# Kernel tuning notes

Hardware: AMD Instinct MI355X
Metric: run time of the kernel (lower is better)

The kernel has to match this reference:

```python
import jax, jax.numpy as jnp
import numpy as np
from jax import lax

EPS = 1e-5
NUM_HEADS = 8


def _safe_norm(x):
    # sqrt(max(sum x^2, EPS^2)) == max(||x||, EPS); grad-safe at 0
    return jnp.sqrt(jnp.maximum(jnp.sum(x * x, axis=-1, keepdims=True), EPS * EPS))


def _project(x):
    norm = _safe_norm(x)
    max_norm = 1.0 - EPS
    scale = jnp.where(norm >= max_norm, max_norm / (norm + EPS), jnp.ones_like(norm))
    return x * scale


def _logmap0(y):
    # logarithmic_map(0, y): lambda_0 = 2/(1+EPS)
    y = _project(y)
    n = _safe_norm(y)  # clamp(min=EPS) is built in
    lam = 2.0 / (1.0 + EPS)
    return (2.0 / lam) * jnp.arctanh(n) * (y / n)


def _expmap0(v):
    # exponential_map(0, v): lambda_0 = 2/(1+EPS)
    n = _safe_norm(v)
    lam = 2.0 / (1.0 + EPS)
    return _project(jnp.tanh(lam * n / 2.0) * (v / n))


def _mobius_add(x, y):
    x = _project(x)
    y = _project(y)
    xy = jnp.sum(x * y, axis=-1, keepdims=True)
    xn = jnp.sum(x * x, axis=-1, keepdims=True)
    yn = jnp.sum(y * y, axis=-1, keepdims=True)
    num = (1.0 + 2.0 * xy + yn) * x + (1.0 - xn) * y
    den = 1.0 + 2.0 * xy + xn * yn + EPS
    return _project(num / den)


def _hyp_linear(x, W, b):
    # HyperbolicLinear.forward: project -> logmap0 -> linear -> expmap0 -> mobius-add bias
    x = _project(x)
    xt = _logmap0(x)
    t = xt @ W.T
    r = _expmap0(t)
    r = _mobius_add(r, jnp.broadcast_to(b, r.shape))
    return r


def setup_inputs() -> dict:
    key = jax.random.key(0)
    ks = jax.random.split(key, 11)
    B, S, E = 4, 512, 512

    def xavier(k, shape):
        bound = np.sqrt(6.0 / (shape[0] + shape[1]))
        return jax.random.uniform(k, shape, jnp.float32, -bound, bound)

    return {
        "query": jax.random.normal(ks[0], (B, S, E), jnp.float32),
        "key": jax.random.normal(ks[1], (B, S, E), jnp.float32),
        "value": jax.random.normal(ks[2], (B, S, E), jnp.float32),
        "Wq": xavier(ks[3], (E, E)), "bq": 0.01 * jax.random.normal(ks[4], (E,), jnp.float32),
        "Wk": xavier(ks[5], (E, E)), "bk": 0.01 * jax.random.normal(ks[6], (E,), jnp.float32),
        "Wv": xavier(ks[7], (E, E)), "bv": 0.01 * jax.random.normal(ks[8], (E,), jnp.float32),
        "Wo": xavier(ks[9], (E, E)), "bo": 0.01 * jax.random.normal(ks[10], (E,), jnp.float32),
    }


def reference(query, key, value, Wq, bq, Wk, bk, Wv, bv, Wo, bo):
    B, S, E = query.shape
    H = NUM_HEADS
    D = E // H

    Q = _hyp_linear(query, Wq, bq).reshape(B, S, H, D).transpose(0, 2, 1, 3)  # [B,H,S,D]
    K = _hyp_linear(key, Wk, bk).reshape(B, S, H, D).transpose(0, 2, 1, 3)
    V = _hyp_linear(value, Wv, bv).reshape(B, S, H, D).transpose(0, 2, 1, 3)

    # Pairwise Poincare distance: d(q,k) = acosh(1 + 2||q-k||^2/((1-|q|^2)(1-|k|^2)) + EPS)
    q = _project(Q)
    k = _project(K)
    qn = jnp.sum(q * q, axis=-1)  # [B,H,S]
    kn = jnp.sum(k * k, axis=-1)  # [B,H,S]
    qk = jnp.einsum('bhqd,bhkd->bhqk', q, k)
    num = jnp.maximum(qn[..., :, None] + kn[..., None, :] - 2.0 * qk, 0.0)
    den = jnp.maximum((1.0 - qn)[..., :, None] * (1.0 - kn)[..., None, :], EPS)
    dist = jnp.arccosh(1.0 + 2.0 * num / den + EPS)  # [B,H,Sq,Sk]
    attn = jax.nn.softmax(-dist, axis=-1)

    # Sequential Mobius-add accumulation over key/value positions
    wt = jnp.moveaxis(attn, 3, 0)  # [Sk,B,H,Sq]
    vt = jnp.moveaxis(V, 2, 0)     # [Sk,B,H,D]

    @jax.checkpoint
    def step(ws, wv):
        wj, vj = wv  # wj: [B,H,Sq], vj: [B,H,D]
        return _mobius_add(ws, wj[..., None] * vj[:, :, None, :]), None

    ws0 = jnp.zeros((B, H, S, D), query.dtype)
    attended, _ = lax.scan(step, ws0, (wt, vt))  # [B,H,Sq,D]

    attended = attended.transpose(0, 2, 1, 3).reshape(B, S, E)
    return _hyp_linear(attended, Wo, bo)
```

## Files before the change

### kernel.cpp

```cpp
#include <hip/hip_runtime.h>
#include <math.h>

#define EPS  1e-5f
#define EPS2 1e-10f
#define MAXN (1.0f - EPS)

using short8  = __attribute__((ext_vector_type(8))) short;
using floatx4 = __attribute__((ext_vector_type(4))) float;
using float2v = __attribute__((ext_vector_type(2))) float;

template <int CTRL>
static __device__ __forceinline__ float qperm(float x) {
  return __int_as_float(__builtin_amdgcn_update_dpp(
      __float_as_int(x), __float_as_int(x), CTRL, 0xF, 0xF, false));
}
#define QP_XOR1    0xB1
#define QP_XOR2    0x4E
#define QP_HALFMIR 0x141

#if __has_builtin(__builtin_elementwise_fma)
static __device__ __forceinline__ float2v fma2(float2v a, float2v b, float2v c) {
  return __builtin_elementwise_fma(a, b, c);
}
#else
static __device__ __forceinline__ float2v fma2(float2v a, float2v b, float2v c) {
  float2v r; r.x = fmaf(a.x, b.x, c.x); r.y = fmaf(a.y, b.y, c.y); return r;
}
#endif

static __device__ __forceinline__ int pack_hi2(float a, float b) {
  return (int)((__float_as_uint(a) >> 16) | (__float_as_uint(b) & 0xFFFF0000u));
}
static __device__ __forceinline__ float hi_of(float a) {
  return __uint_as_float(__float_as_uint(a) & 0xFFFF0000u);
}

static __device__ __forceinline__ float logmap_f(float ss) {
  const float r = sqrtf(fmaxf(ss, EPS2));
  float at;
  if (r >= MAXN) {
    at = 0.5f * logf((r * (2.0f - EPS) + EPS) / (EPS * (1.0f + r)));
  } else {
    at = 0.5f * logf((1.0f + r) / (1.0f - r));
  }
  return (1.0f + EPS) * at / r;
}

__global__ __launch_bounds__(256) void k_gemm_mfma(
    const float* __restrict__ A0, const float* __restrict__ A1, const float* __restrict__ A2,
    const float* __restrict__ W0, const float* __restrict__ W1, const float* __restrict__ W2,
    float* __restrict__ Cbase) {
  const int z = blockIdx.z;
  const float* A = (z == 0) ? A0 : ((z == 1) ? A1 : A2);
  const float* W = (z == 0) ? W0 : ((z == 1) ? W1 : W2);
  float* C = Cbase + (size_t)z * (2048 * 512);
  __shared__ int Ahi[64][36], Alo[64][36], Whi[64][36], Wlo[64][36];
  __shared__ float f_lds[64];
  const int t = threadIdx.x;
  const int n0 = blockIdx.x * 64;
  const int m0 = blockIdx.y * 64;
  const int row = t >> 2, c0 = (t & 3) * 16, ci = (t & 3) * 8;
  const int w = t >> 6, lane = t & 63;
  const int quad = lane >> 4, l16 = lane & 15;
  const int mw = (w & 1) * 32, nw = (w >> 1) * 32;
  floatx4 acc[2][2];
#pragma unroll
  for (int i = 0; i < 2; ++i)
#pragma unroll
    for (int j = 0; j < 2; ++j) acc[i][j] = (floatx4){0.f, 0.f, 0.f, 0.f};
  float ssq = 0.0f;

  for (int k0 = 0; k0 < 512; k0 += 64) {
    float4 av[4], wv[4];
#pragma unroll
    for (int i = 0; i < 4; ++i) {
      av[i] = *(const float4*)&A[(size_t)(n0 + row) * 512 + k0 + c0 + 4 * i];
      wv[i] = *(const float4*)&W[(size_t)(m0 + row) * 512 + k0 + c0 + 4 * i];
    }
    int pAh[8], pAl[8], pWh[8], pWl[8];
#pragma unroll
    for (int i = 0; i < 4; ++i) {
      ssq = fmaf(av[i].x, av[i].x, ssq); ssq = fmaf(av[i].y, av[i].y, ssq);
      ssq = fmaf(av[i].z, av[i].z, ssq); ssq = fmaf(av[i].w, av[i].w, ssq);
      pAh[2 * i]     = pack_hi2(av[i].x, av[i].y);
      pAh[2 * i + 1] = pack_hi2(av[i].z, av[i].w);
      pAl[2 * i]     = pack_hi2(av[i].x - hi_of(av[i].x), av[i].y - hi_of(av[i].y));
      pAl[2 * i + 1] = pack_hi2(av[i].z - hi_of(av[i].z), av[i].w - hi_of(av[i].w));
      pWh[2 * i]     = pack_hi2(wv[i].x, wv[i].y);
      pWh[2 * i + 1] = pack_hi2(wv[i].z, wv[i].w);
      pWl[2 * i]     = pack_hi2(wv[i].x - hi_of(wv[i].x), wv[i].y - hi_of(wv[i].y));
      pWl[2 * i + 1] = pack_hi2(wv[i].z - hi_of(wv[i].z), wv[i].w - hi_of(wv[i].w));
    }
    __syncthreads();
    *(int4*)&Ahi[row][ci]     = *(int4*)&pAh[0];
    *(int4*)&Ahi[row][ci + 4] = *(int4*)&pAh[4];
    *(int4*)&Alo[row][ci]     = *(int4*)&pAl[0];
    *(int4*)&Alo[row][ci + 4] = *(int4*)&pAl[4];
    *(int4*)&Whi[row][ci]     = *(int4*)&pWh[0];
    *(int4*)&Whi[row][ci + 4] = *(int4*)&pWh[4];
    *(int4*)&Wlo[row][ci]     = *(int4*)&pWl[0];
    *(int4*)&Wlo[row][ci + 4] = *(int4*)&pWl[4];
    __syncthreads();
#pragma unroll
    for (int kk = 0; kk < 64; kk += 32) {
      short8 ah[2], al[2], bh[2], bl[2];
#pragma unroll
      for (int i = 0; i < 2; ++i) {
        ah[i] = *(const short8*)&((const short*)Ahi[mw + i * 16 + l16])[kk + quad * 8];
        al[i] = *(const short8*)&((const short*)Alo[mw + i * 16 + l16])[kk + quad * 8];
        bh[i] = *(const short8*)&((const short*)Whi[nw + i * 16 + l16])[kk + quad * 8];
        bl[i] = *(const short8*)&((const short*)Wlo[nw + i * 16 + l16])[kk + quad * 8];
      }
#pragma unroll
      for (int i = 0; i < 2; ++i)
#pragma unroll
        for (int j = 0; j < 2; ++j) {
          acc[i][j] = __builtin_amdgcn_mfma_f32_16x16x32_bf16(ah[i], bh[j], acc[i][j], 0, 0, 0);
          acc[i][j] = __builtin_amdgcn_mfma_f32_16x16x32_bf16(ah[i], bl[j], acc[i][j], 0, 0, 0);
          acc[i][j] = __builtin_amdgcn_mfma_f32_16x16x32_bf16(al[i], bh[j], acc[i][j], 0, 0, 0);
        }
    }
  }
  ssq += qperm<QP_XOR1>(ssq);
  ssq += qperm<QP_XOR2>(ssq);
  if ((t & 3) == 0) f_lds[row] = logmap_f(ssq);
  __syncthreads();
#pragma unroll
  for (int i = 0; i < 2; ++i) {
    const int lrow_base = mw + i * 16 + quad * 4;
#pragma unroll
    for (int r = 0; r < 4; ++r) {
      const float fv = f_lds[lrow_base + r];
#pragma unroll
      for (int j = 0; j < 2; ++j)
        C[(size_t)(n0 + lrow_base + r) * 512 + m0 + nw + j * 16 + l16] = fv * acc[i][j][r];
    }
  }
}

__global__ __launch_bounds__(256) void k_post(const float* __restrict__ tin,
                                              const float* __restrict__ b0,
                                              const float* __restrict__ b1,
                                              const float* __restrict__ b2,
                                              float* __restrict__ o0, float* __restrict__ o1,
                                              float* __restrict__ o2,
                                              float* __restrict__ nrm0, float* __restrict__ nrm1,
                                              float* __restrict__ nrm2,
                                              float* __restrict__ rowsum_init, int final_mode) {
  const int nrow = blockIdx.x, z = blockIdx.y, t = threadIdx.x;
  const float* tv = tin + ((size_t)z * 2048 + nrow) * 512;
  const float* bias = (z == 0) ? b0 : ((z == 1) ? b1 : b2);
  const int e0 = 2 * t;
  const float2 tp = *(const float2*)&tv[e0];
  const float2 bp = *(const float2*)&bias[e0];
  float p_tt = tp.x * tp.x + tp.y * tp.y;
  float p_tb = tp.x * bp.x + tp.y * bp.y;
  float p_bb = bp.x * bp.x + bp.y * bp.y;
#pragma unroll
  for (int m = 32; m; m >>= 1) {
    p_tt += __shfl_xor(p_tt, m, 64);
    p_tb += __shfl_xor(p_tb, m, 64);
    p_bb += __shfl_xor(p_bb, m, 64);
  }
  __shared__ float red[4][3];
  const int lane = t & 63, w = t >> 6;
  if (lane == 0) { red[w][0] = p_tt; red[w][1] = p_tb; red[w][2] = p_bb; }
  __syncthreads();
  const float s_tt = red[0][0] + red[1][0] + red[2][0] + red[3][0];
  const float s_tb = red[0][1] + red[1][1] + red[2][1] + red[3][1];
  const float s_bb = red[0][2] + red[1][2] + red[2][2] + red[3][2];
  const float tn = sqrtf(fmaxf(s_tt, EPS2));
  const float th = tanhf(tn / (1.0f + EPS));
  const float g = th / tn;
  const float rnorm = th * (sqrtf(s_tt) / tn);
  const float sr = (rnorm >= MAXN) ? (MAXN / (rnorm + EPS)) : 1.0f;
  const float gr = g * sr;
  const float rn = (rnorm * sr) * (rnorm * sr);
  const float bnorm = sqrtf(fmaxf(s_bb, EPS2));
  const float sb = (bnorm >= MAXN) ? (MAXN / (bnorm + EPS)) : 1.0f;
  const float xy = gr * sb * s_tb;
  const float yn = (sb * sb) * s_bb;
  const float Af = 1.0f + 2.0f * xy + yn;
  const float Cf = 1.0f - rn;
  const float den = 1.0f + 2.0f * xy + rn * yn + EPS;
  const float id = 1.0f / den;
  const float on_raw = (Af * Af * rn + 2.0f * Af * Cf * xy + Cf * Cf * yn) * (id * id);
  const float no = sqrtf(fmaxf(on_raw, EPS2));
  const float so = (no >= MAXN) ? (MAXN / (no + EPS)) : 1.0f;
  const float ms = id * so;
  const float ca = gr * Af * ms;
  const float cb = sb * Cf * ms;
  const float v0 = ca * tp.x + cb * bp.x;
  const float v1 = ca * tp.y + cb * bp.y;
  if (final_mode) {
    float2 o; o.x = v0; o.y = v1;
    *(float2*)&o0[(size_t)nrow * 512 + e0] = o;
    return;
  }
  float hp = v0 * v0 + v1 * v1;
#pragma unroll
  for (int m = 16; m; m >>= 1) hp += __shfl_xor(hp, m, 64);
  const float hnr = sqrtf(fmaxf(hp, EPS2));
  float sh = 1.0f;
  if (z != 2) sh = (hnr >= MAXN) ? (MAXN / (hnr + EPS)) : 1.0f;
  float* outz = (z == 0) ? o0 : ((z == 1) ? o1 : o2);
  float* nz = (z == 0) ? nrm0 : ((z == 1) ? nrm1 : nrm2);
  const int b = nrow >> 9, s = nrow & 511, h = e0 >> 6, d = e0 & 63;
  float2 o; o.x = v0 * sh; o.y = v1 * sh;
  *(float2*)&outz[(((size_t)(b * 8 + h) * 512 + s) * 64 + d)] = o;
  if ((t & 31) == 0) nz[(size_t)(b * 8 + h) * 512 + s] = hp * sh * sh;
  if (z == 0 && t < 8) rowsum_init[((size_t)(nrow >> 9) * 8 + t) * 512 + (nrow & 511)] = 0.0f;
}

__global__ __launch_bounds__(256) void k_logits(const float* __restrict__ Q,
                                                const float* __restrict__ K,
                                                const float* __restrict__ qn,
                                                const float* __restrict__ kn,
                                                float* __restrict__ attn,
                                                float* __restrict__ rowsum) {
  const int bh = blockIdx.z;
  const int i0 = blockIdx.x * 64;
  const int j0 = blockIdx.y * 64;
  const float* Qb = Q + (size_t)bh * 512 * 64;
  const float* Kb = K + (size_t)bh * 512 * 64;
  __shared__ int Qhi[64][36], Qlo[64][36], Khi[64][36], Klo[64][36];
  const int t = threadIdx.x;
  const int row = t >> 2, c0 = (t & 3) * 16, ci = (t & 3) * 8;
  const int w = t >> 6, lane = t & 63;
  const int quad = lane >> 4, l16 = lane & 15;
  const int mw = (w & 1) * 32, nw = (w >> 1) * 32;
  float4 qv4[4], kv4[4];
#pragma unroll
  for (int i = 0; i < 4; ++i) {
    qv4[i] = *(const float4*)&Qb[(size_t)(i0 + row) * 64 + c0 + 4 * i];
    kv4[i] = *(const float4*)&Kb[(size_t)(j0 + row) * 64 + c0 + 4 * i];
  }
  int pQh[8], pQl[8], pKh[8], pKl[8];
#pragma unroll
  for (int i = 0; i < 4; ++i) {
    pQh[2 * i]     = pack_hi2(qv4[i].x, qv4[i].y);
    pQh[2 * i + 1] = pack_hi2(qv4[i].z, qv4[i].w);
    pQl[2 * i]     = pack_hi2(qv4[i].x - hi_of(qv4[i].x), qv4[i].y - hi_of(qv4[i].y));
    pQl[2 * i + 1] = pack_hi2(qv4[i].z - hi_of(qv4[i].z), qv4[i].w - hi_of(qv4[i].w));
    pKh[2 * i]     = pack_hi2(kv4[i].x, kv4[i].y);
    pKh[2 * i + 1] = pack_hi2(kv4[i].z, kv4[i].w);
    pKl[2 * i]     = pack_hi2(kv4[i].x - hi_of(kv4[i].x), kv4[i].y - hi_of(kv4[i].y));
    pKl[2 * i + 1] = pack_hi2(kv4[i].z - hi_of(kv4[i].z), kv4[i].w - hi_of(kv4[i].w));
  }
  *(int4*)&Qhi[row][ci]     = *(int4*)&pQh[0];
  *(int4*)&Qhi[row][ci + 4] = *(int4*)&pQh[4];
  *(int4*)&Qlo[row][ci]     = *(int4*)&pQl[0];
  *(int4*)&Qlo[row][ci + 4] = *(int4*)&pQl[4];
  *(int4*)&Khi[row][ci]     = *(int4*)&pKh[0];
  *(int4*)&Khi[row][ci + 4] = *(int4*)&pKh[4];
  *(int4*)&Klo[row][ci]     = *(int4*)&pKl[0];
  *(int4*)&Klo[row][ci + 4] = *(int4*)&pKl[4];
  __syncthreads();
  floatx4 acc[2][2];
#pragma unroll
  for (int i = 0; i < 2; ++i)
#pragma unroll
    for (int j = 0; j < 2; ++j) acc[i][j] = (floatx4){0.f, 0.f, 0.f, 0.f};
#pragma unroll
  for (int kk = 0; kk < 64; kk += 32) {
    short8 ah[2], al[2], bhv[2], blv[2];
#pragma unroll
    for (int i = 0; i < 2; ++i) {
      ah[i]  = *(const short8*)&((const short*)Qhi[mw + i * 16 + l16])[kk + quad * 8];
      al[i]  = *(const short8*)&((const short*)Qlo[mw + i * 16 + l16])[kk + quad * 8];
      bhv[i] = *(const short8*)&((const short*)Khi[nw + i * 16 + l16])[kk + quad * 8];
      blv[i] = *(const short8*)&((const short*)Klo[nw + i * 16 + l16])[kk + quad * 8];
    }
#pragma unroll
    for (int i = 0; i < 2; ++i)
#pragma unroll
      for (int j = 0; j < 2; ++j) {
        acc[i][j] = __builtin_amdgcn_mfma_f32_16x16x32_bf16(ah[i], bhv[j], acc[i][j], 0, 0, 0);
        acc[i][j] = __builtin_amdgcn_mfma_f32_16x16x32_bf16(ah[i], blv[j], acc[i][j], 0, 0, 0);
        acc[i][j] = __builtin_amdgcn_mfma_f32_16x16x32_bf16(al[i], bhv[j], acc[i][j], 0, 0, 0);
      }
  }
#pragma unroll
  for (int i = 0; i < 2; ++i) {
    float rs_acc[4] = {0.f, 0.f, 0.f, 0.f};
#pragma unroll
    for (int r = 0; r < 4; ++r) {
      const int grow = i0 + mw + i * 16 + quad * 4 + r;
      const float qni = qn[(size_t)bh * 512 + grow];
      const float rq = 1.0f - qni;
#pragma unroll
      for (int j = 0; j < 2; ++j) {
        const int gcol = j0 + nw + j * 16 + l16;
        const float knj = kn[(size_t)bh * 512 + gcol];
        const float num = fmaxf(qni + knj - 2.0f * acc[i][j][r], 0.0f);
        const float den = fmaxf(rq * (1.0f - knj), EPS);
        const float wv = fmaf(2.0f * num, __builtin_amdgcn_rcpf(den), EPS);
        const float s_ = 1.0f + wv + sqrtf(wv * (wv + 2.0f));
        const float rr = __builtin_amdgcn_rcpf(s_);
        rs_acc[r] += rr;
        attn[((size_t)bh * 512 + grow) * 512 + gcol] = rr;
      }
    }
#pragma unroll
    for (int r = 0; r < 4; ++r) {
      float v = rs_acc[r];
      v += __shfl_xor(v, 1, 64); v += __shfl_xor(v, 2, 64);
      v += __shfl_xor(v, 4, 64); v += __shfl_xor(v, 8, 64);
      if (l16 == 0)
        atomicAdd(&rowsum[(size_t)bh * 512 + i0 + mw + i * 16 + quad * 4 + r], v);
    }
  }
}

__global__ __launch_bounds__(256) void k_scan(const float* __restrict__ V,
                                              const float* __restrict__ vn,
                                              const float* __restrict__ rw,
                                              const float* __restrict__ rowsum,
                                              float* __restrict__ att) {
  __shared__ __align__(16) float v_lds[64 * 64];
  __shared__ __align__(16) float sy_lds[32][132];
  __shared__ __align__(16) float g_lds[256];
  const int blk = blockIdx.x;
  const int bh = blk >> 4;
  const int i0 = (blk & 15) * 32;
  const int t = threadIdx.x;
  const int lane = t & 63, w = t >> 6;
  const int row_blk = w * 8 + (lane >> 3);
  const int sub = lane & 7;
  const int d0 = sub * 8;
  const float* Vb = V + (size_t)bh * 512 * 64;
  const float* vnb = vn + (size_t)bh * 512;
  const float* arow = rw + ((size_t)bh * 512 + i0 + row_blk) * 512;
  const float inv_s = __builtin_amdgcn_rcpf(rowsum[(size_t)bh * 512 + i0 + row_blk]);

  {
    const float* vp = Vb + (size_t)(2 * t) * 64;
    float acc = 0.0f;
#pragma unroll
    for (int i = 0; i < 16; ++i) {
      const float4 x = *(const float4*)&vp[4 * i];
      const float4 y = *(const float4*)&vp[64 + 4 * i];
      acc = fmaf(x.x, y.x, acc); acc = fmaf(x.y, y.y, acc);
      acc = fmaf(x.z, y.z, acc); acc = fmaf(x.w, y.w, acc);
    }
    g_lds[t] = acc;
  }

  float2v wsv[4];
#pragma unroll
  for (int k = 0; k < 4; ++k) wsv[k] = (float2v){0.f, 0.f};
  float xn = 0.0f;

  for (int jc = 0; jc < 512; jc += 64) {
#pragma unroll
    for (int it = 0; it < 4; ++it) {
      const int idx4 = it * 256 + t;
      *(float4*)&v_lds[idx4 * 4] = *(const float4*)&Vb[(size_t)jc * 64 + idx4 * 4];
    }
    const float4 a0 = *(const float4*)&arow[jc + sub * 8];
    const float4 a1 = *(const float4*)&arow[jc + sub * 8 + 4];
    const float4 n0 = *(const float4*)&vnb[jc + sub * 8];
    const float4 n1 = *(const float4*)&vnb[jc + sub * 8 + 4];
    const float wq[8] = {a0.x, a0.y, a0.z, a0.w, a1.x, a1.y, a1.z, a1.w};
    const float nq[8] = {n0.x, n0.y, n0.z, n0.w, n1.x, n1.y, n1.z, n1.w};
#pragma unroll
    for (int k = 0; k < 4; ++k) {
      const float s0 = wq[2 * k] * inv_s;
      const float s1 = wq[2 * k + 1] * inv_s;
      float4 pkt;
      pkt.x = s0; pkt.y = (s0 * s0) * nq[2 * k];
      pkt.z = s1; pkt.w = (s1 * s1) * nq[2 * k + 1];
      *(float4*)&sy_lds[row_blk][sub * 16 + 4 * k] = pkt;
    }
    __syncthreads();

#pragma unroll
    for (int p = 0; p < 32; ++p) {
      const int j = 2 * p;
      const float4 sy4 = *(const float4*)&sy_lds[row_blk][4 * p];
      const float gj = g_lds[(jc >> 1) + p];
      const float4 va0 = *(const float4*)&v_lds[j * 64 + d0];
      const float4 va1 = *(const float4*)&v_lds[j * 64 + d0 + 4];
      const float4 vb0 = *(const float4*)&v_lds[(j + 1) * 64 + d0];
      const float4 vb1 = *(const float4*)&v_lds[(j + 1) * 64 + d0 + 4];
      const float2v a0v = {va0.x, va0.y}, a1v = {va0.z, va0.w};
      const float2v a2v = {va1.x, va1.y}, a3v = {va1.z, va1.w};
      const float2v b0v = {vb0.x, vb0.y}, b1v = {vb0.z, vb0.w};
      const float2v b2v = {vb1.x, vb1.y}, b3v = {vb1.z, vb1.w};
      float2v pa = wsv[0] * a0v; pa = fma2(wsv[1], a1v, pa);
      float2v pb = wsv[2] * a2v; pb = fma2(wsv[3], a3v, pb);
      float2v qa = wsv[0] * b0v; qa = fma2(wsv[1], b1v, qa);
      float2v qb = wsv[2] * b2v; qb = fma2(wsv[3], b3v, qb);
      const float2v ps = pa + pb;
      const float2v qs = qa + qb;
      float dd = ps.x + ps.y;
      float ee = qs.x + qs.y;
      dd += qperm<QP_XOR1>(dd);    ee += qperm<QP_XOR1>(ee);
      dd += qperm<QP_XOR2>(dd);    ee += qperm<QP_XOR2>(ee);
      dd += qperm<QP_HALFMIR>(dd); ee += qperm<QP_HALFMIR>(ee);
      const float sw0 = sy4.x, yn0 = sy4.y;
      const float xy0  = sw0 * dd;
      const float den0 = fmaf(2.0f, xy0, fmaf(xn, yn0, 1.0f + EPS));
      const float s20  = fmaf(2.0f, xy0, xn + yn0);
      const float Af0  = fmaf(2.0f, xy0, 1.0f + yn0);
      const float id0  = __builtin_amdgcn_rcpf(den0);
      const float am0  = Af0 * id0;
      const float cm0  = ((1.0f - xn) * sw0) * id0;
      const float xn1  = (s20 * id0) * ((den0 - EPS) * id0);
      const float sw1 = sy4.z, yn1 = sy4.w;
      const float dd1  = fmaf(am0, ee, cm0 * gj);
      const float xy1  = sw1 * dd1;
      const float den1 = fmaf(2.0f, xy1, fmaf(xn1, yn1, 1.0f + EPS));
      const float s21  = fmaf(2.0f, xy1, xn1 + yn1);
      const float Af1  = fmaf(2.0f, xy1, 1.0f + yn1);
      const float id1  = __builtin_amdgcn_rcpf(den1);
      const float am1  = Af1 * id1;
      const float cm1  = ((1.0f - xn1) * sw1) * id1;
      xn = (s21 * id1) * ((den1 - EPS) * id1);
      const float A2 = am1 * am0, Bc = am1 * cm0;
      const float2v A2v = {A2, A2}, Bv = {Bc, Bc}, Cv = {cm1, cm1};
      wsv[0] = fma2(A2v, wsv[0], fma2(Bv, a0v, Cv * b0v));
      wsv[1] = fma2(A2v, wsv[1], fma2(Bv, a1v, Cv * b1v));
      wsv[2] = fma2(A2v, wsv[2], fma2(Bv, a2v, Cv * b2v));
      wsv[3] = fma2(A2v, wsv[3], fma2(Bv, a3v, Cv * b3v));
    }
    __syncthreads();
  }
  const int b = bh >> 3, h = bh & 7;
  float* o = att + (((size_t)b * 512 + i0 + row_blk) * 512 + h * 64 + d0);
  float4 s0; s0.x = wsv[0].x; s0.y = wsv[0].y; s0.z = wsv[1].x; s0.w = wsv[1].y;
  float4 s1; s1.x = wsv[2].x; s1.y = wsv[2].y; s1.z = wsv[3].x; s1.w = wsv[3].y;
  *(float4*)&o[0] = s0;
  *(float4*)&o[4] = s1;
}

extern "C" void kernel_launch(void* const* d_in, const int* in_sizes, int n_in,
                              void* d_out, int out_size, void* d_ws, size_t ws_size,
                              hipStream_t stream) {
  const float* query = (const float*)d_in[0];
  const float* key_  = (const float*)d_in[1];
  const float* value = (const float*)d_in[2];
  const float* Wq = (const float*)d_in[3];
  const float* bq = (const float*)d_in[4];
  const float* Wk = (const float*)d_in[5];
  const float* bk = (const float*)d_in[6];
  const float* Wv = (const float*)d_in[7];
  const float* bv = (const float*)d_in[8];
  const float* Wo = (const float*)d_in[9];
  const float* bo = (const float*)d_in[10];
  float* ws = (float*)d_ws;
  const size_t M = 1u << 20;
  float* Qb     = ws;
  float* Kb     = ws + 1 * M;
  float* Vb     = ws + 2 * M;
  float* qn     = ws + 3 * M;
  float* kn     = qn + 16384;
  float* vn     = kn + 16384;
  float* rowsum = vn + 16384;
  float* rw     = ws + 4 * M;
  float* t3     = ws + 12 * M;
  float* att    = ws + 15 * M;
  float* to_    = ws + 16 * M;

  k_gemm_mfma<<<dim3(32, 8, 3), 256, 0, stream>>>(query, key_, value, Wq, Wk, Wv, t3);
  k_post<<<dim3(2048, 3), 256, 0, stream>>>(t3, bq, bk, bv, Qb, Kb, Vb, qn, kn, vn,
                                            rowsum, 0);
  k_logits<<<dim3(8, 8, 32), 256, 0, stream>>>(Qb, Kb, qn, kn, rw, rowsum);
  k_scan<<<512, 256, 0, stream>>>(Vb, vn, rw, rowsum, att);
  k_gemm_mfma<<<dim3(32, 8, 1), 256, 0, stream>>>(att, att, att, Wo, Wo, Wo, to_);
  k_post<<<dim3(2048, 1), 256, 0, stream>>>(to_, bo, bo, bo, (float*)d_out,
                                            nullptr, nullptr, nullptr, nullptr, nullptr,
                                            nullptr, 1);
}
```

Before: 247.1 us.

## Block the Mobius scan four steps at a time using in-chunk Gram dot products

The sequential Mobius-add scan now advances four key positions per iteration instead of two. The four dot products with the running state are computed up front and reduced in one batch of DPP shuffles, then corrected step by step using pairwise V Gram entries that are built in LDS for each chunk. The old global-memory precompute of adjacent-pair dots is replaced by a per-chunk computation on 96 threads, which adds a barrier. The goal is fewer cross-lane reduction rounds and more instruction-level parallelism along the serial dependency chain, at the cost of more registers and a longer scalar recurrence per step.

```diff
diff --git a/kernel.cpp b/kernel.cpp
--- a/kernel.cpp
+++ b/kernel.cpp
@@ -318,8 +318,8 @@
                                               const float* __restrict__ rowsum,
                                               float* __restrict__ att) {
   __shared__ __align__(16) float v_lds[64 * 64];
-  __shared__ __align__(16) float sy_lds[32][132];
-  __shared__ __align__(16) float g_lds[256];
+  __shared__ __align__(16) float sy_lds[32 * 132];
+  __shared__ __align__(16) float g_lds[16 * 8];
   const int blk = blockIdx.x;
   const int bh = blk >> 4;
   const int i0 = (blk & 15) * 32;
@@ -333,19 +333,6 @@
   const float* arow = rw + ((size_t)bh * 512 + i0 + row_blk) * 512;
   const float inv_s = __builtin_amdgcn_rcpf(rowsum[(size_t)bh * 512 + i0 + row_blk]);
 
-  {
-    const float* vp = Vb + (size_t)(2 * t) * 64;
-    float acc = 0.0f;
-#pragma unroll
-    for (int i = 0; i < 16; ++i) {
-      const float4 x = *(const float4*)&vp[4 * i];
-      const float4 y = *(const float4*)&vp[64 + 4 * i];
-      acc = fmaf(x.x, y.x, acc); acc = fmaf(x.y, y.y, acc);
-      acc = fmaf(x.z, y.z, acc); acc = fmaf(x.w, y.w, acc);
-    }
-    g_lds[t] = acc;
-  }
-
   float2v wsv[4];
 #pragma unroll
   for (int k = 0; k < 4; ++k) wsv[k] = (float2v){0.f, 0.f};
@@ -357,72 +344,143 @@
       const int idx4 = it * 256 + t;
       *(float4*)&v_lds[idx4 * 4] = *(const float4*)&Vb[(size_t)jc * 64 + idx4 * 4];
     }
-    const float4 a0 = *(const float4*)&arow[jc + sub * 8];
-    const float4 a1 = *(const float4*)&arow[jc + sub * 8 + 4];
-    const float4 n0 = *(const float4*)&vnb[jc + sub * 8];
-    const float4 n1 = *(const float4*)&vnb[jc + sub * 8 + 4];
-    const float wq[8] = {a0.x, a0.y, a0.z, a0.w, a1.x, a1.y, a1.z, a1.w};
-    const float nq[8] = {n0.x, n0.y, n0.z, n0.w, n1.x, n1.y, n1.z, n1.w};
-#pragma unroll
-    for (int k = 0; k < 4; ++k) {
-      const float s0 = wq[2 * k] * inv_s;
-      const float s1 = wq[2 * k + 1] * inv_s;
-      float4 pkt;
-      pkt.x = s0; pkt.y = (s0 * s0) * nq[2 * k];
-      pkt.z = s1; pkt.w = (s1 * s1) * nq[2 * k + 1];
-      *(float4*)&sy_lds[row_blk][sub * 16 + 4 * k] = pkt;
+    {
+      const float4 a0 = *(const float4*)&arow[jc + sub * 8];
+      const float4 a1 = *(const float4*)&arow[jc + sub * 8 + 4];
+      const float4 n0 = *(const float4*)&vnb[jc + sub * 8];
+      const float4 n1 = *(const float4*)&vnb[jc + sub * 8 + 4];
+      const float s0 = a0.x * inv_s, s1 = a0.y * inv_s, s2_ = a0.z * inv_s, s3 = a0.w * inv_s;
+      const float s4 = a1.x * inv_s, s5 = a1.y * inv_s, s6 = a1.z * inv_s, s7 = a1.w * inv_s;
+      float4 p0, p1, p2, p3;
+      p0.x = s0;  p0.y = (s0 * s0) * n0.x;  p0.z = s1;  p0.w = (s1 * s1) * n0.y;
+      p1.x = s2_; p1.y = (s2_ * s2_) * n0.z; p1.z = s3; p1.w = (s3 * s3) * n0.w;
+      p2.x = s4;  p2.y = (s4 * s4) * n1.x;  p2.z = s5;  p2.w = (s5 * s5) * n1.y;
+      p3.x = s6;  p3.y = (s6 * s6) * n1.z;  p3.z = s7;  p3.w = (s7 * s7) * n1.w;
+      const int base = row_blk * 132 + 16 * sub;
+      *(float4*)&sy_lds[base]      = p0;
+      *(float4*)&sy_lds[base + 4]  = p1;
+      *(float4*)&sy_lds[base + 8]  = p2;
+      *(float4*)&sy_lds[base + 12] = p3;
     }
     __syncthreads();
-
-#pragma unroll
-    for (int p = 0; p < 32; ++p) {
-      const int j = 2 * p;
-      const float4 sy4 = *(const float4*)&sy_lds[row_blk][4 * p];
-      const float gj = g_lds[(jc >> 1) + p];
+    if (t < 96) {
+      const int c = t / 6, pi = t - 6 * c;
+      const int kk = (pi < 3) ? 0 : ((pi < 5) ? 1 : 2);
+      const int jj = (pi < 3) ? (pi + 1) : ((pi < 5) ? (pi - 2) : 3);
+      const float* va = &v_lds[(4 * c + kk) * 64];
+      const float* vb = &v_lds[(4 * c + jj) * 64];
+      float acc = 0.0f;
+#pragma unroll
+      for (int i = 0; i < 16; ++i) {
+        const float4 x = *(const float4*)&va[4 * i];
+        const float4 y = *(const float4*)&vb[4 * i];
+        acc = fmaf(x.x, y.x, acc); acc = fmaf(x.y, y.y, acc);
+        acc = fmaf(x.z, y.z, acc); acc = fmaf(x.w, y.w, acc);
+      }
+      g_lds[c * 8 + pi] = acc;
+    }
+    __syncthreads();
+
+    for (int c = 0; c < 16; ++c) {
+      const int j = 4 * c;
+      const float4 sy_a = *(const float4*)&sy_lds[row_blk * 132 + 8 * c];
+      const float4 sy_b = *(const float4*)&sy_lds[row_blk * 132 + 8 * c + 4];
+      const float4 g_a = *(const float4*)&g_lds[c * 8];
+      const float4 g_b = *(const float4*)&g_lds[c * 8 + 4];
       const float4 va0 = *(const float4*)&v_lds[j * 64 + d0];
       const float4 va1 = *(const float4*)&v_lds[j * 64 + d0 + 4];
       const float4 vb0 = *(const float4*)&v_lds[(j + 1) * 64 + d0];
       const float4 vb1 = *(const float4*)&v_lds[(j + 1) * 64 + d0 + 4];
+      const float4 vc0 = *(const float4*)&v_lds[(j + 2) * 64 + d0];
+      const float4 vc1 = *(const float4*)&v_lds[(j + 2) * 64 + d0 + 4];
+      const float4 vd0 = *(const float4*)&v_lds[(j + 3) * 64 + d0];
+      const float4 vd1 = *(const float4*)&v_lds[(j + 3) * 64 + d0 + 4];
       const float2v a0v = {va0.x, va0.y}, a1v = {va0.z, va0.w};
       const float2v a2v = {va1.x, va1.y}, a3v = {va1.z, va1.w};
       const float2v b0v = {vb0.x, vb0.y}, b1v = {vb0.z, vb0.w};
       const float2v b2v = {vb1.x, vb1.y}, b3v = {vb1.z, vb1.w};
+      const float2v c0v = {vc0.x, vc0.y}, c1v = {vc0.z, vc0.w};
+      const float2v c2v = {vc1.x, vc1.y}, c3v = {vc1.z, vc1.w};
+      const float2v d0v = {vd0.x, vd0.y}, d1v = {vd0.z, vd0.w};
+      const float2v d2v = {vd1.x, vd1.y}, d3v = {vd1.z, vd1.w};
       float2v pa = wsv[0] * a0v; pa = fma2(wsv[1], a1v, pa);
       float2v pb = wsv[2] * a2v; pb = fma2(wsv[3], a3v, pb);
+      const float2v sva = pa + pb;
+      float p0 = sva.x + sva.y;
       float2v qa = wsv[0] * b0v; qa = fma2(wsv[1], b1v, qa);
       float2v qb = wsv[2] * b2v; qb = fma2(wsv[3], b3v, qb);
-      const float2v ps = pa + pb;
-      const float2v qs = qa + qb;
-      float dd = ps.x + ps.y;
-      float ee = qs.x + qs.y;
-      dd += qperm<QP_XOR1>(dd);    ee += qperm<QP_XOR1>(ee);
-      dd += qperm<QP_XOR2>(dd);    ee += qperm<QP_XOR2>(ee);
-      dd += qperm<QP_HALFMIR>(dd); ee += qperm<QP_HALFMIR>(ee);
-      const float sw0 = sy4.x, yn0 = sy4.y;
-      const float xy0  = sw0 * dd;
-      const float den0 = fmaf(2.0f, xy0, fmaf(xn, yn0, 1.0f + EPS));
-      const float s20  = fmaf(2.0f, xy0, xn + yn0);
-      const float Af0  = fmaf(2.0f, xy0, 1.0f + yn0);
-      const float id0  = __builtin_amdgcn_rcpf(den0);
-      const float am0  = Af0 * id0;
-      const float cm0  = ((1.0f - xn) * sw0) * id0;
-      const float xn1  = (s20 * id0) * ((den0 - EPS) * id0);
-      const float sw1 = sy4.z, yn1 = sy4.w;
-      const float dd1  = fmaf(am0, ee, cm0 * gj);
-      const float xy1  = sw1 * dd1;
-      const float den1 = fmaf(2.0f, xy1, fmaf(xn1, yn1, 1.0f + EPS));
-      const float s21  = fmaf(2.0f, xy1, xn1 + yn1);
-      const float Af1  = fmaf(2.0f, xy1, 1.0f + yn1);
-      const float id1  = __builtin_amdgcn_rcpf(den1);
-      const float am1  = Af1 * id1;
-      const float cm1  = ((1.0f - xn1) * sw1) * id1;
-      xn = (s21 * id1) * ((den1 - EPS) * id1);
-      const float A2 = am1 * am0, Bc = am1 * cm0;
-      const float2v A2v = {A2, A2}, Bv = {Bc, Bc}, Cv = {cm1, cm1};
-      wsv[0] = fma2(A2v, wsv[0], fma2(Bv, a0v, Cv * b0v));
-      wsv[1] = fma2(A2v, wsv[1], fma2(Bv, a1v, Cv * b1v));
-      wsv[2] = fma2(A2v, wsv[2], fma2(Bv, a2v, Cv * b2v));
-      wsv[3] = fma2(A2v, wsv[3], fma2(Bv, a3v, Cv * b3v));
+      const float2v svb = qa + qb;
+      float p1 = svb.x + svb.y;
+      float2v ra = wsv[0] * c0v; ra = fma2(wsv[1], c1v, ra);
+      float2v rb = wsv[2] * c2v; rb = fma2(wsv[3], c3v, rb);
+      const float2v svc = ra + rb;
+      float p2 = svc.x + svc.y;
+      float2v sa = wsv[0] * d0v; sa = fma2(wsv[1], d1v, sa);
+      float2v sb = wsv[2] * d2v; sb = fma2(wsv[3], d3v, sb);
+      const float2v svd = sa + sb;
+      float p3 = svd.x + svd.y;
+      p0 += qperm<QP_XOR1>(p0); p1 += qperm<QP_XOR1>(p1);
+      p2 += qperm<QP_XOR1>(p2); p3 += qperm<QP_XOR1>(p3);
+      p0 += qperm<QP_XOR2>(p0); p1 += qperm<QP_XOR2>(p1);
+      p2 += qperm<QP_XOR2>(p2); p3 += qperm<QP_XOR2>(p3);
+      p0 += qperm<QP_HALFMIR>(p0); p1 += qperm<QP_HALFMIR>(p1);
+      p2 += qperm<QP_HALFMIR>(p2); p3 += qperm<QP_HALFMIR>(p3);
+      float e1 = p1, e2 = p2, e3 = p3;
+      const float sw0 = sy_a.x, yn0 = sy_a.y;
+      float xy  = sw0 * p0;
+      float den = fmaf(2.0f, xy, fmaf(xn, yn0, 1.0f + EPS));
+      float s2  = fmaf(2.0f, xy, xn + yn0);
+      float Af  = fmaf(2.0f, xy, 1.0f + yn0);
+      float id  = __builtin_amdgcn_rcpf(den);
+      const float am0 = Af * id;
+      const float cm0 = ((1.0f - xn) * sw0) * id;
+      xn = (s2 * id) * ((den - EPS) * id);
+      e1 = fmaf(am0, e1, cm0 * g_a.x);
+      e2 = fmaf(am0, e2, cm0 * g_a.y);
+      e3 = fmaf(am0, e3, cm0 * g_a.z);
+      const float sw1 = sy_a.z, yn1 = sy_a.w;
+      xy  = sw1 * e1;
+      den = fmaf(2.0f, xy, fmaf(xn, yn1, 1.0f + EPS));
+      s2  = fmaf(2.0f, xy, xn + yn1);
+      Af  = fmaf(2.0f, xy, 1.0f + yn1);
+      id  = __builtin_amdgcn_rcpf(den);
+      const float am1 = Af * id;
+      const float cm1 = ((1.0f - xn) * sw1) * id;
+      xn = (s2 * id) * ((den - EPS) * id);
+      e2 = fmaf(am1, e2, cm1 * g_a.w);
+      e3 = fmaf(am1, e3, cm1 * g_b.x);
+      const float sw2 = sy_b.x, yn2 = sy_b.y;
+      xy  = sw2 * e2;
+      den = fmaf(2.0f, xy, fmaf(xn, yn2, 1.0f + EPS));
+      s2  = fmaf(2.0f, xy, xn + yn2);
+      Af  = fmaf(2.0f, xy, 1.0f + yn2);
+      id  = __builtin_amdgcn_rcpf(den);
+      const float am2 = Af * id;
+      const float cm2 = ((1.0f - xn) * sw2) * id;
+      xn = (s2 * id) * ((den - EPS) * id);
+      e3 = fmaf(am2, e3, cm2 * g_b.y);
+      const float sw3 = sy_b.z, yn3 = sy_b.w;
+      xy  = sw3 * e3;
+      den = fmaf(2.0f, xy, fmaf(xn, yn3, 1.0f + EPS));
+      s2  = fmaf(2.0f, xy, xn + yn3);
+      Af  = fmaf(2.0f, xy, 1.0f + yn3);
+      id  = __builtin_amdgcn_rcpf(den);
+      const float am3 = Af * id;
+      const float cm3 = ((1.0f - xn) * sw3) * id;
+      xn = (s2 * id) * ((den - EPS) * id);
+      const float t32  = am3 * am2;
+      const float B2c  = am3 * cm2;
+      const float B3c  = cm3;
+      const float B1c  = t32 * cm1;
+      const float t321 = t32 * am1;
+      const float B0c  = t321 * cm0;
+      const float Ac   = t321 * am0;
+      const float2v Av = {Ac, Ac}, B0v2 = {B0c, B0c}, B1v2 = {B1c, B1c};
+      const float2v B2v2 = {B2c, B2c}, B3v2 = {B3c, B3c};
+      wsv[0] = fma2(Av, wsv[0], fma2(B0v2, a0v, fma2(B1v2, b0v, fma2(B2v2, c0v, B3v2 * d0v))));
+      wsv[1] = fma2(Av, wsv[1], fma2(B0v2, a1v, fma2(B1v2, b1v, fma2(B2v2, c1v, B3v2 * d1v))));
+      wsv[2] = fma2(Av, wsv[2], fma2(B0v2, a2v, fma2(B1v2, b2v, fma2(B2v2, c2v, B3v2 * d2v))));
+      wsv[3] = fma2(Av, wsv[3], fma2(B0v2, a3v, fma2(B1v2, b3v, fma2(B2v2, c3v, B3v2 * d3v))));
     }
     __syncthreads();
   }
```

Measured after the change: 245.5 us. About the same (-0.6%).
